# Kernel optimization log

Measured on AMD Instinct MI355X. Metric: run time of the kernel, lower is better.

Reference implementation:

```python
import jax, jax.numpy as jnp
import numpy as np

DIM = 1024
D_STATE = 16
D_CONV = 4
EXPAND = 2
D_INNER = EXPAND * DIM
BATCH = 4
SEQ = 2048


def setup_inputs() -> dict:
    key = jax.random.key(0)
    ks = jax.random.split(key, 9)
    n = lambda i, shape, scale=0.02: (jax.random.normal(ks[i], shape, jnp.float32) * scale)
    return {
        "x": jax.random.normal(ks[0], (BATCH, SEQ, DIM), jnp.float32),
        "in_proj_w": n(1, (D_INNER, DIM)),
        "conv_w": n(2, (D_INNER, D_CONV), 0.1),          # depthwise kernel (groups=d_inner)
        "x_proj_w": n(3, (2 * D_STATE + 1, D_INNER)),
        "dt_proj_w": n(4, (D_INNER, 1), 1.0),
        "dt_proj_b": n(5, (D_INNER,), 0.1),
        "A_log": jax.random.normal(ks[6], (D_INNER, D_STATE), jnp.float32),
        "D": jnp.ones((D_INNER,), jnp.float32),
        "out_proj_w": n(7, (DIM, D_INNER)),
        "norm_w": jnp.ones((DIM,), jnp.float32),
        "norm_b": jnp.zeros((DIM,), jnp.float32),
    }


def reference(x, in_proj_w, conv_w, x_proj_w, dt_proj_w, dt_proj_b,
              A_log, D, out_proj_w, norm_w, norm_b):
    Bsz, L, _ = x.shape
    shortcut = x

    # LayerNorm
    mu = jnp.mean(x, axis=-1, keepdims=True)
    var = jnp.var(x, axis=-1, keepdims=True)
    h = (x - mu) / jnp.sqrt(var + 1e-5) * norm_w + norm_b

    # in_proj: [B,L,dim] -> [B,L,d_inner]
    h = h @ in_proj_w.T

    # causal depthwise conv1d (padding d_conv-1, truncate to L)
    hp = jnp.pad(h, ((0, 0), (D_CONV - 1, 0), (0, 0)))
    h_conv = sum(hp[:, k:k + L, :] * conv_w[:, k] for k in range(D_CONV))
    h = jax.nn.silu(h_conv)

    # x_proj -> dt (1), B (d_state), C (d_state)
    proj = h @ x_proj_w.T
    dt_in = proj[..., :1]
    B_param = proj[..., 1:1 + D_STATE]      # [B,L,d_state]
    C_param = proj[..., 1 + D_STATE:]       # [B,L,d_state]
    dt = jax.nn.softplus(dt_in @ dt_proj_w.T + dt_proj_b)  # [B,L,d_inner]

    A = -jnp.exp(A_log)                     # [d_inner, d_state]

    def step(state, inp):
        dt_t, B_t, C_t, x_t = inp           # [B,d_inner],[B,ds],[B,ds],[B,d_inner]
        state = jnp.exp(A[None] * dt_t[:, :, None]) * state \
                + B_t[:, None, :] * x_t[:, :, None]          # [B,d_inner,d_state]
        y = jnp.einsum('bnd,bd->bn', state, C_t) + D * x_t   # [B,d_inner]
        return state, y

    init = jnp.zeros((Bsz, D_INNER, D_STATE), x.dtype)
    xs = (jnp.swapaxes(dt, 0, 1), jnp.swapaxes(B_param, 0, 1),
          jnp.swapaxes(C_param, 0, 1), jnp.swapaxes(h, 0, 1))
    state, ys = jax.lax.scan(step, init, xs)
    y = jnp.swapaxes(ys, 0, 1)              # [B,L,d_inner]

    out = jax.nn.silu(y) @ out_proj_w.T + shortcut
    return out, state
```

## Files before the change

### kernel.cpp

```cpp
#include <hip/hip_runtime.h>

typedef unsigned short u16;
typedef unsigned int u32;
typedef __attribute__((ext_vector_type(8))) short short8;
typedef __attribute__((ext_vector_type(4))) float f32x4;
typedef __attribute__((ext_vector_type(8))) unsigned short ushort8_t;

#define SEQ 2048
#define DIM 1024
#define DINNER 2048
#define NPROJ 33
#define NPROJ_PAD 48
#define LC 32
#define NC 64

__device__ __forceinline__ u16 f2bf(float f) {
  union { float f; u32 u; } v; v.f = f;
  u32 r = (v.u + 0x7fffu + ((v.u >> 16) & 1u)) >> 16;
  return (u16)r;
}
__device__ __forceinline__ float bf2f(u16 s) {
  union { u32 u; float f; } v; v.u = ((u32)s) << 16;
  return v.f;
}
__device__ __forceinline__ float fexp2(float x) {
#if __has_builtin(__builtin_amdgcn_exp2f)
  return __builtin_amdgcn_exp2f(x);
#else
  return __expf(x * 0.69314718f);
#endif
}
__device__ __forceinline__ float softplus(float x) {
  return fmaxf(x, 0.f) + __logf(1.f + __expf(-fabsf(x)));
}
__device__ __forceinline__ void async16(const void* g, void* l) {
  __builtin_amdgcn_global_load_lds(
      (const __attribute__((address_space(1))) u32*)g,
      (__attribute__((address_space(3))) u32*)l, 16, 0, 0);
}

__global__ void cast_w_kernel(const float* __restrict__ w1, const float* __restrict__ w3,
                              u16* __restrict__ o1, u16* __restrict__ o3) {
  int i = blockIdx.x * 256 + threadIdx.x;
  float4 a = ((const float4*)w1)[i];
  float4 b = ((const float4*)w3)[i];
  ushort4 oa, ob;
  oa.x = f2bf(a.x); oa.y = f2bf(a.y); oa.z = f2bf(a.z); oa.w = f2bf(a.w);
  ob.x = f2bf(b.x); ob.y = f2bf(b.y); ob.z = f2bf(b.z); ob.w = f2bf(b.w);
  ((ushort4*)o1)[i] = oa;
  ((ushort4*)o3)[i] = ob;
}

__global__ void cast_w2pad_kernel(const float* __restrict__ src, u16* __restrict__ dst) {
  int i = blockIdx.x * 256 + threadIdx.x;
  int j = i >> 11, k = i & 2047;
  dst[i] = (j < NPROJ) ? f2bf(src[j * 2048 + k]) : (u16)0;
}

__global__ __launch_bounds__(256) void ln_kernel(const float* __restrict__ x,
                                                 const float* __restrict__ w,
                                                 const float* __restrict__ b,
                                                 u16* __restrict__ h) {
  const int row = blockIdx.x;
  const int tid = threadIdx.x;
  const int lane = tid & 63, wave = tid >> 6;
  const float4 v = ((const float4*)(x + (size_t)row * DIM))[tid];
  float s = v.x + v.y + v.z + v.w;
  float q = v.x * v.x + v.y * v.y + v.z * v.z + v.w * v.w;
  for (int off = 32; off; off >>= 1) {
    s += __shfl_down(s, off);
    q += __shfl_down(q, off);
  }
  __shared__ float sbuf[8];
  if (lane == 0) { sbuf[wave] = s; sbuf[4 + wave] = q; }
  __syncthreads();
  float tot = sbuf[0] + sbuf[1] + sbuf[2] + sbuf[3];
  float totq = sbuf[4] + sbuf[5] + sbuf[6] + sbuf[7];
  const float mean = tot * (1.0f / DIM);
  const float var = totq * (1.0f / DIM) - mean * mean;
  const float rs = rsqrtf(var + 1e-5f);
  const float4 wv = ((const float4*)w)[tid];
  const float4 bv = ((const float4*)b)[tid];
  ushort4 o;
  o.x = f2bf((v.x - mean) * rs * wv.x + bv.x);
  o.y = f2bf((v.y - mean) * rs * wv.y + bv.y);
  o.z = f2bf((v.z - mean) * rs * wv.z + bv.z);
  o.w = f2bf((v.w - mean) * rs * wv.w + bv.w);
  ((ushort4*)(h + (size_t)row * DIM))[tid] = o;
}

__global__ __launch_bounds__(256) void gemm_bf16_kernel(const u16* __restrict__ A,
                                                        const u16* __restrict__ Bt,
                                                        u16* __restrict__ C,
                                                        int K, int N) {
  __shared__ u16 As[128 * 32];
  __shared__ u16 Bs[128 * 32];
  const int tid = threadIdx.x;
  const int lane = tid & 63, wave = tid >> 6;
  const int wm = wave >> 1, wn = wave & 1;
  const int row16 = lane & 15, quad = lane >> 4;
  const int bn = blockIdx.x, bm = blockIdx.y;
  f32x4 acc[4][4] = {};
  const u16* Ablk = A + (size_t)bm * 128 * K;
  const u16* Bblk = Bt + (size_t)bn * 128 * K;
  for (int k0 = 0; k0 < K; k0 += 32) {
#pragma unroll
    for (int i = 0; i < 2; ++i) {
      int c = tid + i * 256;
      int r = c >> 2, cc = (c & 3) * 8;
      async16(Ablk + (size_t)r * K + k0 + cc, &As[c * 8]);
      async16(Bblk + (size_t)r * K + k0 + cc, &Bs[c * 8]);
    }
    __syncthreads();
    short8 af[4], bfr[4];
#pragma unroll
    for (int i = 0; i < 4; ++i) {
      af[i] = *(const short8*)&As[(wm * 64 + i * 16 + row16) * 32 + quad * 8];
      bfr[i] = *(const short8*)&Bs[(wn * 64 + i * 16 + row16) * 32 + quad * 8];
    }
#pragma unroll
    for (int i = 0; i < 4; ++i)
#pragma unroll
      for (int j = 0; j < 4; ++j)
        acc[i][j] = __builtin_amdgcn_mfma_f32_16x16x32_bf16(af[i], bfr[j], acc[i][j], 0, 0, 0);
    __syncthreads();
  }
#pragma unroll
  for (int i = 0; i < 4; ++i) {
    int m = bm * 128 + wm * 64 + i * 16 + quad * 4;
#pragma unroll
    for (int j = 0; j < 4; ++j) {
      int n = bn * 128 + wn * 64 + j * 16 + row16;
#pragma unroll
      for (int r = 0; r < 4; ++r)
        C[(size_t)(m + r) * N + n] = f2bf(acc[i][j][r]);
    }
  }
}

__global__ __launch_bounds__(256) void gemm_out_kernel(const u16* __restrict__ A,
                                                       const u16* __restrict__ Bt,
                                                       const float* __restrict__ resid,
                                                       float* __restrict__ C,
                                                       int K, int N) {
  __shared__ u16 As[128 * 32];
  __shared__ u16 Bs[128 * 32];
  const int tid = threadIdx.x;
  const int lane = tid & 63, wave = tid >> 6;
  const int wm = wave >> 1, wn = wave & 1;
  const int row16 = lane & 15, quad = lane >> 4;
  const int bn = blockIdx.x, bm = blockIdx.y;
  f32x4 acc[4][4] = {};
  const u16* Ablk = A + (size_t)bm * 128 * K;
  const u16* Bblk = Bt + (size_t)bn * 128 * K;
  for (int k0 = 0; k0 < K; k0 += 32) {
#pragma unroll
    for (int i = 0; i < 2; ++i) {
      int c = tid + i * 256;
      int r = c >> 2, cc = (c & 3) * 8;
      async16(Ablk + (size_t)r * K + k0 + cc, &As[c * 8]);
      async16(Bblk + (size_t)r * K + k0 + cc, &Bs[c * 8]);
    }
    __syncthreads();
    short8 af[4], bfr[4];
#pragma unroll
    for (int i = 0; i < 4; ++i) {
      af[i] = *(const short8*)&As[(wm * 64 + i * 16 + row16) * 32 + quad * 8];
      bfr[i] = *(const short8*)&Bs[(wn * 64 + i * 16 + row16) * 32 + quad * 8];
    }
#pragma unroll
    for (int i = 0; i < 4; ++i)
#pragma unroll
      for (int j = 0; j < 4; ++j)
        acc[i][j] = __builtin_amdgcn_mfma_f32_16x16x32_bf16(af[i], bfr[j], acc[i][j], 0, 0, 0);
    __syncthreads();
  }
#pragma unroll
  for (int i = 0; i < 4; ++i) {
    int m = bm * 128 + wm * 64 + i * 16 + quad * 4;
#pragma unroll
    for (int j = 0; j < 4; ++j) {
      int n = bn * 128 + wn * 64 + j * 16 + row16;
#pragma unroll
      for (int r = 0; r < 4; ++r) {
        size_t idx = (size_t)(m + r) * N + n;
        C[idx] = acc[i][j][r] + resid[idx];
      }
    }
  }
}

__global__ __launch_bounds__(256) void conv_silu_kernel(const u16* __restrict__ c1,
                                                        const float* __restrict__ cw,
                                                        u16* __restrict__ cs) {
  const int tid = threadIdx.x;
  const int dg = tid * 8;
  const size_t m0 = (size_t)blockIdx.x * 8;
  const int l0 = (int)(m0 & (SEQ - 1));
  float w[4][8];
  {
    const float4* cw4 = (const float4*)(cw + (size_t)dg * 4);
#pragma unroll
    for (int c = 0; c < 8; ++c) {
      float4 v = cw4[c];
      w[0][c] = v.x; w[1][c] = v.y; w[2][c] = v.z; w[3][c] = v.w;
    }
  }
  const u16* base = c1 + m0 * DINNER + dg;
  ushort8_t win0, win1, win2, win3;
  const ushort8_t zero = (ushort8_t)0;
  if (l0 == 0) {
    win0 = zero; win1 = zero; win2 = zero;
  } else {
    win0 = *(const ushort8_t*)(base - 3 * DINNER);
    win1 = *(const ushort8_t*)(base - 2 * DINNER);
    win2 = *(const ushort8_t*)(base - 1 * DINNER);
  }
  win3 = *(const ushort8_t*)(base);
#pragma unroll
  for (int t = 0; t < 8; ++t) {
    ushort8_t nxt = win3;
    if (t < 7) nxt = *(const ushort8_t*)(base + (size_t)(t + 1) * DINNER);
    ushort8_t o;
#pragma unroll
    for (int c = 0; c < 8; ++c) {
      float acc = bf2f((u16)win0[c]) * w[0][c];
      acc = fmaf(bf2f((u16)win1[c]), w[1][c], acc);
      acc = fmaf(bf2f((u16)win2[c]), w[2][c], acc);
      acc = fmaf(bf2f((u16)win3[c]), w[3][c], acc);
      const float s = acc / (1.f + __expf(-acc));
      o[c] = (unsigned short)f2bf(s);
    }
    *(ushort8_t*)(cs + (m0 + t) * DINNER + dg) = o;
    win0 = win1; win1 = win2; win2 = win3; win3 = nxt;
  }
}

__global__ __launch_bounds__(256) void gemm_w2_kernel(const u16* __restrict__ A,
                                                      const u16* __restrict__ Bt,
                                                      float* __restrict__ C) {
  __shared__ u16 As[128 * 32];
  __shared__ u16 Bs[48 * 32];
  const int tid = threadIdx.x;
  const int lane = tid & 63, wave = tid >> 6;
  const int row16 = lane & 15, quad = lane >> 4;
  const int bm = blockIdx.x;
  const int K = DINNER;
  f32x4 acc[2][3] = {};
  const u16* Ablk = A + (size_t)bm * 128 * K;
  for (int k0 = 0; k0 < K; k0 += 32) {
#pragma unroll
    for (int i = 0; i < 2; ++i) {
      int c = tid + i * 256;
      int r = c >> 2, cc = (c & 3) * 8;
      async16(Ablk + (size_t)r * K + k0 + cc, &As[c * 8]);
    }
    if (tid < 192) {
      int c = tid;
      int r = c >> 2, cc = (c & 3) * 8;
      async16(Bt + (size_t)r * K + k0 + cc, &Bs[c * 8]);
    }
    __syncthreads();
    short8 af[2], bfr[3];
#pragma unroll
    for (int i = 0; i < 2; ++i)
      af[i] = *(const short8*)&As[(wave * 32 + i * 16 + row16) * 32 + quad * 8];
#pragma unroll
    for (int j = 0; j < 3; ++j)
      bfr[j] = *(const short8*)&Bs[(j * 16 + row16) * 32 + quad * 8];
#pragma unroll
    for (int i = 0; i < 2; ++i)
#pragma unroll
      for (int j = 0; j < 3; ++j)
        acc[i][j] = __builtin_amdgcn_mfma_f32_16x16x32_bf16(af[i], bfr[j], acc[i][j], 0, 0, 0);
    __syncthreads();
  }
#pragma unroll
  for (int i = 0; i < 2; ++i) {
    int m = bm * 128 + wave * 32 + i * 16 + quad * 4;
#pragma unroll
    for (int j = 0; j < 3; ++j) {
      int n = j * 16 + row16;
#pragma unroll
      for (int r = 0; r < 4; ++r)
        C[(size_t)(m + r) * NPROJ_PAD + n] = acc[i][j][r];
    }
  }
}


__global__ __launch_bounds__(256) void scan_phase1(const float* __restrict__ proj,
                                                   const u16* __restrict__ xs,
                                                   const float* __restrict__ dtw_,
                                                   const float* __restrict__ dtb_,
                                                   const float* __restrict__ A_log,
                                                   u16* __restrict__ S,
                                                   float* __restrict__ Tdt) {
  __shared__ float Bs[LC][16];
  __shared__ float DTin[LC];
  const int tid = threadIdx.x;
  const int d = blockIdx.x * 256 + tid;
  const int c = blockIdx.y;
  const int b = blockIdx.z;
  const size_t mrow = (size_t)b * SEQ + c * LC;
  for (int i = tid; i < LC * 16; i += 256) {
    int t = i >> 4, n = i & 15;
    Bs[t][n] = proj[(mrow + t) * NPROJ_PAD + 1 + n];
  }
  if (tid < LC) DTin[tid] = proj[(mrow + tid) * NPROJ_PAD];
  __syncthreads();
  float An2[16];
#pragma unroll
  for (int n = 0; n < 16; ++n) An2[n] = -__expf(A_log[d * 16 + n]) * 1.44269504f;
  const float dtw = dtw_[d], dtb = dtb_[d];
  float s[16];
#pragma unroll
  for (int n = 0; n < 16; ++n) s[n] = 0.f;
  float Tsum = 0.f;
  const u16* xp = xs + mrow * DINNER + d;
  u16 xnext = *xp;
#pragma unroll 2
  for (int t = 0; t < LC; ++t) {
    const float xv = bf2f(xnext);
    if (t + 1 < LC) xnext = xp[(size_t)(t + 1) * DINNER];
    const float sp = softplus(fmaf(DTin[t], dtw, dtb));
    Tsum += sp;
    const float4 B0 = *(const float4*)&Bs[t][0];
    const float4 B1 = *(const float4*)&Bs[t][4];
    const float4 B2 = *(const float4*)&Bs[t][8];
    const float4 B3 = *(const float4*)&Bs[t][12];
    const float bb[16] = {B0.x, B0.y, B0.z, B0.w, B1.x, B1.y, B1.z, B1.w,
                          B2.x, B2.y, B2.z, B2.w, B3.x, B3.y, B3.z, B3.w};
#pragma unroll
    for (int n = 0; n < 16; ++n)
      s[n] = fmaf(fexp2(An2[n] * sp), s[n], bb[n] * xv);
  }
  const size_t so = ((size_t)(b * NC + c) * DINNER + d) * 16;
  ushort8_t o0, o1;
#pragma unroll
  for (int j = 0; j < 8; ++j) {
    o0[j] = (unsigned short)f2bf(s[j]);
    o1[j] = (unsigned short)f2bf(s[8 + j]);
  }
  *(ushort8_t*)(S + so) = o0;
  *(ushort8_t*)(S + so + 8) = o1;
  Tdt[(size_t)(b * NC + c) * DINNER + d] = Tsum;
}

__global__ __launch_bounds__(256) void scan_phase2(const float* __restrict__ A_log,
                                                   u16* __restrict__ S,
                                                   const float* __restrict__ Tdt,
                                                   float* __restrict__ out_state) {
  const int idx = blockIdx.x * 256 + threadIdx.x;
  const int nq = idx & 3;
  const int d = (idx >> 2) & (DINNER - 1);
  const int b = idx >> 13;
  float An2[4];
#pragma unroll
  for (int n = 0; n < 4; ++n) An2[n] = -__expf(A_log[d * 16 + nq * 4 + n]) * 1.44269504f;
  float prev[4] = {0.f, 0.f, 0.f, 0.f};
  for (int c = 0; c < NC; ++c) {
    const size_t base = (size_t)(b * NC + c) * DINNER + d;
    const float T = Tdt[base];
    const size_t so = base * 16 + nq * 4;
    ushort4 lv = *(const ushort4*)(S + so);
    const float loc[4] = {bf2f(lv.x), bf2f(lv.y), bf2f(lv.z), bf2f(lv.w)};
    ushort4 pv;
    pv.x = f2bf(prev[0]); pv.y = f2bf(prev[1]); pv.z = f2bf(prev[2]); pv.w = f2bf(prev[3]);
    *(ushort4*)(S + so) = pv;
    const float dk = fexp2(An2[0] * T), dk1 = fexp2(An2[1] * T);
    const float dk2 = fexp2(An2[2] * T), dk3 = fexp2(An2[3] * T);
    prev[0] = fmaf(dk, prev[0], loc[0]);
    prev[1] = fmaf(dk1, prev[1], loc[1]);
    prev[2] = fmaf(dk2, prev[2], loc[2]);
    prev[3] = fmaf(dk3, prev[3], loc[3]);
  }
  *(float4*)(out_state + ((size_t)b * DINNER + d) * 16 + nq * 4) =
      make_float4(prev[0], prev[1], prev[2], prev[3]);
}

__global__ __launch_bounds__(256) void scan_phase3(const float* __restrict__ proj,
                                                   const u16* __restrict__ xs,
                                                   const float* __restrict__ dtw_,
                                                   const float* __restrict__ dtb_,
                                                   const float* __restrict__ A_log,
                                                   const float* __restrict__ Dp,
                                                   const u16* __restrict__ S,
                                                   u16* __restrict__ ysil) {
  __shared__ float Bs[LC][16];
  __shared__ float Cs[LC][16];
  __shared__ float DTin[LC];
  const int tid = threadIdx.x;
  const int d = blockIdx.x * 256 + tid;
  const int c = blockIdx.y;
  const int b = blockIdx.z;
  const size_t mrow = (size_t)b * SEQ + c * LC;
  for (int i = tid; i < LC * 16; i += 256) {
    int t = i >> 4, n = i & 15;
    Bs[t][n] = proj[(mrow + t) * NPROJ_PAD + 1 + n];
    Cs[t][n] = proj[(mrow + t) * NPROJ_PAD + 17 + n];
  }
  if (tid < LC) DTin[tid] = proj[(mrow + tid) * NPROJ_PAD];
  __syncthreads();
  float An2[16];
#pragma unroll
  for (int n = 0; n < 16; ++n) An2[n] = -__expf(A_log[d * 16 + n]) * 1.44269504f;
  const float dtw = dtw_[d], dtb = dtb_[d], Dd = Dp[d];
  float s[16];
  const size_t so = ((size_t)(b * NC + c) * DINNER + d) * 16;
  {
    ushort8_t v0 = *(const ushort8_t*)(S + so);
    ushort8_t v1 = *(const ushort8_t*)(S + so + 8);
#pragma unroll
    for (int j = 0; j < 8; ++j) {
      s[j] = bf2f((u16)v0[j]);
      s[8 + j] = bf2f((u16)v1[j]);
    }
  }
  const u16* xp = xs + mrow * DINNER + d;
  u16* yp = ysil + mrow * DINNER + d;
  u16 xnext = *xp;
#pragma unroll 2
  for (int t = 0; t < LC; ++t) {
    const float xv = bf2f(xnext);
    if (t + 1 < LC) xnext = xp[(size_t)(t + 1) * DINNER];
    const float sp = softplus(fmaf(DTin[t], dtw, dtb));
    const float4 B0 = *(const float4*)&Bs[t][0];
    const float4 B1 = *(const float4*)&Bs[t][4];
    const float4 B2 = *(const float4*)&Bs[t][8];
    const float4 B3 = *(const float4*)&Bs[t][12];
    const float bb[16] = {B0.x, B0.y, B0.z, B0.w, B1.x, B1.y, B1.z, B1.w,
                          B2.x, B2.y, B2.z, B2.w, B3.x, B3.y, B3.z, B3.w};
#pragma unroll
    for (int n = 0; n < 16; ++n)
      s[n] = fmaf(fexp2(An2[n] * sp), s[n], bb[n] * xv);
    const float4 C0 = *(const float4*)&Cs[t][0];
    const float4 C1 = *(const float4*)&Cs[t][4];
    const float4 C2 = *(const float4*)&Cs[t][8];
    const float4 C3 = *(const float4*)&Cs[t][12];
    const float cc[16] = {C0.x, C0.y, C0.z, C0.w, C1.x, C1.y, C1.z, C1.w,
                          C2.x, C2.y, C2.z, C2.w, C3.x, C3.y, C3.z, C3.w};
    float y = Dd * xv;
#pragma unroll
    for (int n = 0; n < 16; ++n) y = fmaf(cc[n], s[n], y);
    const float sy = y / (1.f + __expf(-y));
    yp[(size_t)t * DINNER] = f2bf(sy);
  }
}

extern "C" void kernel_launch(void* const* d_in, const int* in_sizes, int n_in,
                              void* d_out, int out_size, void* d_ws, size_t ws_size,
                              hipStream_t stream) {
  const float* x = (const float*)d_in[0];
  const float* in_proj_w = (const float*)d_in[1];
  const float* conv_w = (const float*)d_in[2];
  const float* x_proj_w = (const float*)d_in[3];
  const float* dt_proj_w = (const float*)d_in[4];
  const float* dt_proj_b = (const float*)d_in[5];
  const float* A_log = (const float*)d_in[6];
  const float* Dvec = (const float*)d_in[7];
  const float* out_proj_w = (const float*)d_in[8];
  const float* norm_w = (const float*)d_in[9];
  const float* norm_b = (const float*)d_in[10];

  char* ws = (char*)d_ws;
  u16* h = (u16*)(ws + 0);
  u16* w1b = (u16*)(ws + 16777216);
  u16* w3b = (u16*)(ws + 20971520);
  u16* w2b = (u16*)(ws + 25165824);
  u16* c1 = (u16*)(ws + 25362432);
  u16* ysil = c1;
  u16* cs = (u16*)(ws + 58916864);
  float* proj = (float*)(ws + 92471296);
  u16* Sbuf = (u16*)(ws + 94044160);
  float* Tdt = (float*)(ws + 110821376);

  float* out = (float*)d_out;
  float* out_state = out + (size_t)4 * SEQ * DIM;

  cast_w_kernel<<<2048, 256, 0, stream>>>(in_proj_w, out_proj_w, w1b, w3b);
  cast_w2pad_kernel<<<384, 256, 0, stream>>>(x_proj_w, w2b);
  ln_kernel<<<8192, 256, 0, stream>>>(x, norm_w, norm_b, h);
  gemm_bf16_kernel<<<dim3(DINNER / 128, 64), 256, 0, stream>>>(h, w1b, c1, DIM, DINNER);
  conv_silu_kernel<<<1024, 256, 0, stream>>>(c1, conv_w, cs);
  gemm_w2_kernel<<<64, 256, 0, stream>>>(cs, w2b, proj);
  scan_phase1<<<dim3(DINNER / 256, NC, 4), 256, 0, stream>>>(proj, cs, dt_proj_w, dt_proj_b,
                                                             A_log, Sbuf, Tdt);
  scan_phase2<<<128, 256, 0, stream>>>(A_log, Sbuf, Tdt, out_state);
  scan_phase3<<<dim3(DINNER / 256, NC, 4), 256, 0, stream>>>(proj, cs, dt_proj_w, dt_proj_b,
                                                             A_log, Dvec, Sbuf, ysil);
  gemm_out_kernel<<<dim3(DIM / 128, 64), 256, 0, stream>>>(ysil, w3b, x, out, DINNER, DIM);
}
```

Baseline: 395.4 us.

## Use 8-wave GEMM blocks, smaller x_proj tiles, and packed two-channel scan

The two large bf16 GEMMs now run 512 threads (8 waves) per 128x128 tile, each wave owning a 64x32 sub-tile. Each thread loads a single 16-byte chunk per stage, which is meant to improve latency hiding and occupancy. The skinny x_proj GEMM drops to 64-row tiles, doubling its block count to fill more CUs. The scan phase 1 and 3 kernels now handle two adjacent channels per thread with packed f32x2 FMAs and 32-bit paired bf16 loads and stores, which halves the number of blocks but aims to improve ALU throughput and memory access width.

Result: faster. 385.2 us (-2.6%).

```diff
diff --git a/kernel.cpp b/kernel.cpp
--- a/kernel.cpp
+++ b/kernel.cpp
@@ -4,6 +4,7 @@
 typedef unsigned int u32;
 typedef __attribute__((ext_vector_type(8))) short short8;
 typedef __attribute__((ext_vector_type(4))) float f32x4;
+typedef __attribute__((ext_vector_type(2))) float f32x2;
 typedef __attribute__((ext_vector_type(8))) unsigned short ushort8_t;
 
 #define SEQ 2048
@@ -23,6 +24,12 @@
   union { u32 u; float f; } v; v.u = ((u32)s) << 16;
   return v.f;
 }
+__device__ __forceinline__ float lo_bf(u32 w) {
+  union { u32 u; float f; } v; v.u = w << 16; return v.f;
+}
+__device__ __forceinline__ float hi_bf(u32 w) {
+  union { u32 u; float f; } v; v.u = w & 0xffff0000u; return v.f;
+}
 __device__ __forceinline__ float fexp2(float x) {
 #if __has_builtin(__builtin_amdgcn_exp2f)
   return __builtin_amdgcn_exp2f(x);
@@ -32,6 +39,10 @@
 }
 __device__ __forceinline__ float softplus(float x) {
   return fmaxf(x, 0.f) + __logf(1.f + __expf(-fabsf(x)));
+}
+__device__ __forceinline__ f32x2 sp2(float v) { f32x2 r; r.x = v; r.y = v; return r; }
+__device__ __forceinline__ f32x2 pkfma(f32x2 a, f32x2 b, f32x2 c) {
+  return __builtin_elementwise_fma(a, b, c);
 }
 __device__ __forceinline__ void async16(const void* g, void* l) {
   __builtin_amdgcn_global_load_lds(
@@ -89,7 +100,7 @@
   ((ushort4*)(h + (size_t)row * DIM))[tid] = o;
 }
 
-__global__ __launch_bounds__(256) void gemm_bf16_kernel(const u16* __restrict__ A,
+__global__ __launch_bounds__(512) void gemm_bf16_kernel(const u16* __restrict__ A,
                                                         const u16* __restrict__ Bt,
                                                         u16* __restrict__ C,
                                                         int K, int N) {
@@ -97,31 +108,28 @@
   __shared__ u16 Bs[128 * 32];
   const int tid = threadIdx.x;
   const int lane = tid & 63, wave = tid >> 6;
-  const int wm = wave >> 1, wn = wave & 1;
+  const int wm = wave >> 2, wn = wave & 3;
   const int row16 = lane & 15, quad = lane >> 4;
   const int bn = blockIdx.x, bm = blockIdx.y;
-  f32x4 acc[4][4] = {};
+  f32x4 acc[4][2] = {};
   const u16* Ablk = A + (size_t)bm * 128 * K;
   const u16* Bblk = Bt + (size_t)bn * 128 * K;
+  const int r = tid >> 2, cc = (tid & 3) * 8;
   for (int k0 = 0; k0 < K; k0 += 32) {
-#pragma unroll
-    for (int i = 0; i < 2; ++i) {
-      int c = tid + i * 256;
-      int r = c >> 2, cc = (c & 3) * 8;
-      async16(Ablk + (size_t)r * K + k0 + cc, &As[c * 8]);
-      async16(Bblk + (size_t)r * K + k0 + cc, &Bs[c * 8]);
-    }
+    async16(Ablk + (size_t)r * K + k0 + cc, &As[tid * 8]);
+    async16(Bblk + (size_t)r * K + k0 + cc, &Bs[tid * 8]);
     __syncthreads();
-    short8 af[4], bfr[4];
-#pragma unroll
-    for (int i = 0; i < 4; ++i) {
+    short8 af[4], bfr[2];
+#pragma unroll
+    for (int i = 0; i < 4; ++i)
       af[i] = *(const short8*)&As[(wm * 64 + i * 16 + row16) * 32 + quad * 8];
-      bfr[i] = *(const short8*)&Bs[(wn * 64 + i * 16 + row16) * 32 + quad * 8];
-    }
+#pragma unroll
+    for (int j = 0; j < 2; ++j)
+      bfr[j] = *(const short8*)&Bs[(wn * 32 + j * 16 + row16) * 32 + quad * 8];
 #pragma unroll
     for (int i = 0; i < 4; ++i)
 #pragma unroll
-      for (int j = 0; j < 4; ++j)
+      for (int j = 0; j < 2; ++j)
         acc[i][j] = __builtin_amdgcn_mfma_f32_16x16x32_bf16(af[i], bfr[j], acc[i][j], 0, 0, 0);
     __syncthreads();
   }
@@ -129,16 +137,16 @@
   for (int i = 0; i < 4; ++i) {
     int m = bm * 128 + wm * 64 + i * 16 + quad * 4;
 #pragma unroll
-    for (int j = 0; j < 4; ++j) {
-      int n = bn * 128 + wn * 64 + j * 16 + row16;
-#pragma unroll
-      for (int r = 0; r < 4; ++r)
-        C[(size_t)(m + r) * N + n] = f2bf(acc[i][j][r]);
-    }
-  }
-}
-
-__global__ __launch_bounds__(256) void gemm_out_kernel(const u16* __restrict__ A,
+    for (int j = 0; j < 2; ++j) {
+      int n = bn * 128 + wn * 32 + j * 16 + row16;
+#pragma unroll
+      for (int rr = 0; rr < 4; ++rr)
+        C[(size_t)(m + rr) * N + n] = f2bf(acc[i][j][rr]);
+    }
+  }
+}
+
+__global__ __launch_bounds__(512) void gemm_out_kernel(const u16* __restrict__ A,
                                                        const u16* __restrict__ Bt,
                                                        const float* __restrict__ resid,
                                                        float* __restrict__ C,
@@ -147,31 +155,28 @@
   __shared__ u16 Bs[128 * 32];
   const int tid = threadIdx.x;
   const int lane = tid & 63, wave = tid >> 6;
-  const int wm = wave >> 1, wn = wave & 1;
+  const int wm = wave >> 2, wn = wave & 3;
   const int row16 = lane & 15, quad = lane >> 4;
   const int bn = blockIdx.x, bm = blockIdx.y;
-  f32x4 acc[4][4] = {};
+  f32x4 acc[4][2] = {};
   const u16* Ablk = A + (size_t)bm * 128 * K;
   const u16* Bblk = Bt + (size_t)bn * 128 * K;
+  const int r = tid >> 2, cc = (tid & 3) * 8;
   for (int k0 = 0; k0 < K; k0 += 32) {
-#pragma unroll
-    for (int i = 0; i < 2; ++i) {
-      int c = tid + i * 256;
-      int r = c >> 2, cc = (c & 3) * 8;
-      async16(Ablk + (size_t)r * K + k0 + cc, &As[c * 8]);
-      async16(Bblk + (size_t)r * K + k0 + cc, &Bs[c * 8]);
-    }
+    async16(Ablk + (size_t)r * K + k0 + cc, &As[tid * 8]);
+    async16(Bblk + (size_t)r * K + k0 + cc, &Bs[tid * 8]);
     __syncthreads();
-    short8 af[4], bfr[4];
-#pragma unroll
-    for (int i = 0; i < 4; ++i) {
+    short8 af[4], bfr[2];
+#pragma unroll
+    for (int i = 0; i < 4; ++i)
       af[i] = *(const short8*)&As[(wm * 64 + i * 16 + row16) * 32 + quad * 8];
-      bfr[i] = *(const short8*)&Bs[(wn * 64 + i * 16 + row16) * 32 + quad * 8];
-    }
+#pragma unroll
+    for (int j = 0; j < 2; ++j)
+      bfr[j] = *(const short8*)&Bs[(wn * 32 + j * 16 + row16) * 32 + quad * 8];
 #pragma unroll
     for (int i = 0; i < 4; ++i)
 #pragma unroll
-      for (int j = 0; j < 4; ++j)
+      for (int j = 0; j < 2; ++j)
         acc[i][j] = __builtin_amdgcn_mfma_f32_16x16x32_bf16(af[i], bfr[j], acc[i][j], 0, 0, 0);
     __syncthreads();
   }
@@ -179,12 +184,12 @@
   for (int i = 0; i < 4; ++i) {
     int m = bm * 128 + wm * 64 + i * 16 + quad * 4;
 #pragma unroll
-    for (int j = 0; j < 4; ++j) {
-      int n = bn * 128 + wn * 64 + j * 16 + row16;
-#pragma unroll
-      for (int r = 0; r < 4; ++r) {
-        size_t idx = (size_t)(m + r) * N + n;
-        C[idx] = acc[i][j][r] + resid[idx];
+    for (int j = 0; j < 2; ++j) {
+      int n = bn * 128 + wn * 32 + j * 16 + row16;
+#pragma unroll
+      for (int rr = 0; rr < 4; ++rr) {
+        size_t idx = (size_t)(m + rr) * N + n;
+        C[idx] = acc[i][j][rr] + resid[idx];
       }
     }
   }
@@ -239,52 +244,37 @@
 __global__ __launch_bounds__(256) void gemm_w2_kernel(const u16* __restrict__ A,
                                                       const u16* __restrict__ Bt,
                                                       float* __restrict__ C) {
-  __shared__ u16 As[128 * 32];
+  __shared__ u16 As[64 * 32];
   __shared__ u16 Bs[48 * 32];
   const int tid = threadIdx.x;
   const int lane = tid & 63, wave = tid >> 6;
   const int row16 = lane & 15, quad = lane >> 4;
   const int bm = blockIdx.x;
   const int K = DINNER;
-  f32x4 acc[2][3] = {};
-  const u16* Ablk = A + (size_t)bm * 128 * K;
+  f32x4 acc[3] = {};
+  const u16* Ablk = A + (size_t)bm * 64 * K;
+  const int r = tid >> 2, cc = (tid & 3) * 8;
   for (int k0 = 0; k0 < K; k0 += 32) {
-#pragma unroll
-    for (int i = 0; i < 2; ++i) {
-      int c = tid + i * 256;
-      int r = c >> 2, cc = (c & 3) * 8;
-      async16(Ablk + (size_t)r * K + k0 + cc, &As[c * 8]);
-    }
-    if (tid < 192) {
-      int c = tid;
-      int r = c >> 2, cc = (c & 3) * 8;
-      async16(Bt + (size_t)r * K + k0 + cc, &Bs[c * 8]);
-    }
+    async16(Ablk + (size_t)r * K + k0 + cc, &As[tid * 8]);
+    if (tid < 192) async16(Bt + (size_t)r * K + k0 + cc, &Bs[tid * 8]);
     __syncthreads();
-    short8 af[2], bfr[3];
-#pragma unroll
-    for (int i = 0; i < 2; ++i)
-      af[i] = *(const short8*)&As[(wave * 32 + i * 16 + row16) * 32 + quad * 8];
+    short8 af = *(const short8*)&As[(wave * 16 + row16) * 32 + quad * 8];
+    short8 bfr[3];
 #pragma unroll
     for (int j = 0; j < 3; ++j)
       bfr[j] = *(const short8*)&Bs[(j * 16 + row16) * 32 + quad * 8];
 #pragma unroll
-    for (int i = 0; i < 2; ++i)
-#pragma unroll
-      for (int j = 0; j < 3; ++j)
-        acc[i][j] = __builtin_amdgcn_mfma_f32_16x16x32_bf16(af[i], bfr[j], acc[i][j], 0, 0, 0);
+    for (int j = 0; j < 3; ++j)
+      acc[j] = __builtin_amdgcn_mfma_f32_16x16x32_bf16(af, bfr[j], acc[j], 0, 0, 0);
     __syncthreads();
   }
-#pragma unroll
-  for (int i = 0; i < 2; ++i) {
-    int m = bm * 128 + wave * 32 + i * 16 + quad * 4;
-#pragma unroll
-    for (int j = 0; j < 3; ++j) {
-      int n = j * 16 + row16;
-#pragma unroll
-      for (int r = 0; r < 4; ++r)
-        C[(size_t)(m + r) * NPROJ_PAD + n] = acc[i][j][r];
-    }
+  const int m = bm * 64 + wave * 16 + quad * 4;
+#pragma unroll
+  for (int j = 0; j < 3; ++j) {
+    const int n = j * 16 + row16;
+#pragma unroll
+    for (int rr = 0; rr < 4; ++rr)
+      C[(size_t)(m + rr) * NPROJ_PAD + n] = acc[j][rr];
   }
 }
 
@@ -296,55 +286,66 @@
                                                    const float* __restrict__ A_log,
                                                    u16* __restrict__ S,
                                                    float* __restrict__ Tdt) {
-  __shared__ float Bs[LC][16];
+  __shared__ float Bsh[LC][16];
   __shared__ float DTin[LC];
   const int tid = threadIdx.x;
-  const int d = blockIdx.x * 256 + tid;
+  const int d0 = blockIdx.x * 512 + tid * 2;
   const int c = blockIdx.y;
   const int b = blockIdx.z;
   const size_t mrow = (size_t)b * SEQ + c * LC;
   for (int i = tid; i < LC * 16; i += 256) {
     int t = i >> 4, n = i & 15;
-    Bs[t][n] = proj[(mrow + t) * NPROJ_PAD + 1 + n];
+    Bsh[t][n] = proj[(mrow + t) * NPROJ_PAD + 1 + n];
   }
   if (tid < LC) DTin[tid] = proj[(mrow + tid) * NPROJ_PAD];
   __syncthreads();
-  float An2[16];
-#pragma unroll
-  for (int n = 0; n < 16; ++n) An2[n] = -__expf(A_log[d * 16 + n]) * 1.44269504f;
-  const float dtw = dtw_[d], dtb = dtb_[d];
-  float s[16];
-#pragma unroll
-  for (int n = 0; n < 16; ++n) s[n] = 0.f;
-  float Tsum = 0.f;
-  const u16* xp = xs + mrow * DINNER + d;
-  u16 xnext = *xp;
+  f32x2 An2[16];
+#pragma unroll
+  for (int n = 0; n < 16; ++n) {
+    An2[n].x = -__expf(A_log[(size_t)d0 * 16 + n]) * 1.44269504f;
+    An2[n].y = -__expf(A_log[(size_t)(d0 + 1) * 16 + n]) * 1.44269504f;
+  }
+  const float2 dtwv = *(const float2*)(dtw_ + d0);
+  const float2 dtbv = *(const float2*)(dtb_ + d0);
+  f32x2 dtw2; dtw2.x = dtwv.x; dtw2.y = dtwv.y;
+  f32x2 dtb2; dtb2.x = dtbv.x; dtb2.y = dtbv.y;
+  f32x2 s[16];
+#pragma unroll
+  for (int n = 0; n < 16; ++n) s[n] = sp2(0.f);
+  f32x2 Tsum = sp2(0.f);
+  const u16* xp = xs + mrow * DINNER + d0;
+  u32 xw = *(const u32*)xp;
 #pragma unroll 2
   for (int t = 0; t < LC; ++t) {
-    const float xv = bf2f(xnext);
-    if (t + 1 < LC) xnext = xp[(size_t)(t + 1) * DINNER];
-    const float sp = softplus(fmaf(DTin[t], dtw, dtb));
+    f32x2 xv; xv.x = lo_bf(xw); xv.y = hi_bf(xw);
+    if (t + 1 < LC) xw = *(const u32*)(xp + (size_t)(t + 1) * DINNER);
+    f32x2 dtv = pkfma(sp2(DTin[t]), dtw2, dtb2);
+    f32x2 sp; sp.x = softplus(dtv.x); sp.y = softplus(dtv.y);
     Tsum += sp;
-    const float4 B0 = *(const float4*)&Bs[t][0];
-    const float4 B1 = *(const float4*)&Bs[t][4];
-    const float4 B2 = *(const float4*)&Bs[t][8];
-    const float4 B3 = *(const float4*)&Bs[t][12];
-    const float bb[16] = {B0.x, B0.y, B0.z, B0.w, B1.x, B1.y, B1.z, B1.w,
-                          B2.x, B2.y, B2.z, B2.w, B3.x, B3.y, B3.z, B3.w};
-#pragma unroll
-    for (int n = 0; n < 16; ++n)
-      s[n] = fmaf(fexp2(An2[n] * sp), s[n], bb[n] * xv);
-  }
-  const size_t so = ((size_t)(b * NC + c) * DINNER + d) * 16;
-  ushort8_t o0, o1;
+    const float4* Br = (const float4*)&Bsh[t][0];
+#pragma unroll
+    for (int q = 0; q < 4; ++q) {
+      const float4 Bq = Br[q];
+      const float bqa[4] = {Bq.x, Bq.y, Bq.z, Bq.w};
+#pragma unroll
+      for (int j = 0; j < 4; ++j) {
+        const int n = q * 4 + j;
+        f32x2 e = An2[n] * sp;
+        f32x2 dk; dk.x = fexp2(e.x); dk.y = fexp2(e.y);
+        s[n] = pkfma(dk, s[n], sp2(bqa[j]) * xv);
+      }
+    }
+  }
+  const size_t so = ((size_t)(b * NC + c) * DINNER + d0) * 16;
+  ushort8_t o0, o1, o2, o3;
 #pragma unroll
   for (int j = 0; j < 8; ++j) {
-    o0[j] = (unsigned short)f2bf(s[j]);
-    o1[j] = (unsigned short)f2bf(s[8 + j]);
-  }
-  *(ushort8_t*)(S + so) = o0;
-  *(ushort8_t*)(S + so + 8) = o1;
-  Tdt[(size_t)(b * NC + c) * DINNER + d] = Tsum;
+    o0[j] = f2bf(s[j].x);     o1[j] = f2bf(s[8 + j].x);
+    o2[j] = f2bf(s[j].y);     o3[j] = f2bf(s[8 + j].y);
+  }
+  *(ushort8_t*)(S + so) = o0;       *(ushort8_t*)(S + so + 8) = o1;
+  *(ushort8_t*)(S + so + 16) = o2;  *(ushort8_t*)(S + so + 24) = o3;
+  *(float2*)(Tdt + (size_t)(b * NC + c) * DINNER + d0) = make_float2(Tsum.x, Tsum.y);
 }
 
 __global__ __launch_bounds__(256) void scan_phase2(const float* __restrict__ A_log,
@@ -368,9 +369,9 @@
     ushort4 pv;
     pv.x = f2bf(prev[0]); pv.y = f2bf(prev[1]); pv.z = f2bf(prev[2]); pv.w = f2bf(prev[3]);
     *(ushort4*)(S + so) = pv;
-    const float dk = fexp2(An2[0] * T), dk1 = fexp2(An2[1] * T);
+    const float dk0 = fexp2(An2[0] * T), dk1 = fexp2(An2[1] * T);
     const float dk2 = fexp2(An2[2] * T), dk3 = fexp2(An2[3] * T);
-    prev[0] = fmaf(dk, prev[0], loc[0]);
+    prev[0] = fmaf(dk0, prev[0], loc[0]);
     prev[1] = fmaf(dk1, prev[1], loc[1]);
     prev[2] = fmaf(dk2, prev[2], loc[2]);
     prev[3] = fmaf(dk3, prev[3], loc[3]);
@@ -387,64 +388,77 @@
                                                    const float* __restrict__ Dp,
                                                    const u16* __restrict__ S,
                                                    u16* __restrict__ ysil) {
-  __shared__ float Bs[LC][16];
-  __shared__ float Cs[LC][16];
+  __shared__ float Bsh[LC][16];
+  __shared__ float Csh[LC][16];
   __shared__ float DTin[LC];
   const int tid = threadIdx.x;
-  const int d = blockIdx.x * 256 + tid;
+  const int d0 = blockIdx.x * 512 + tid * 2;
   const int c = blockIdx.y;
   const int b = blockIdx.z;
   const size_t mrow = (size_t)b * SEQ + c * LC;
   for (int i = tid; i < LC * 16; i += 256) {
     int t = i >> 4, n = i & 15;
-    Bs[t][n] = proj[(mrow + t) * NPROJ_PAD + 1 + n];
-    Cs[t][n] = proj[(mrow + t) * NPROJ_PAD + 17 + n];
+    Bsh[t][n] = proj[(mrow + t) * NPROJ_PAD + 1 + n];
+    Csh[t][n] = proj[(mrow + t) * NPROJ_PAD + 17 + n];
   }
   if (tid < LC) DTin[tid] = proj[(mrow + tid) * NPROJ_PAD];
   __syncthreads();
-  float An2[16];
-#pragma unroll
-  for (int n = 0; n < 16; ++n) An2[n] = -__expf(A_log[d * 16 + n]) * 1.44269504f;
-  const float dtw = dtw_[d], dtb = dtb_[d], Dd = Dp[d];
-  float s[16];
-  const size_t so = ((size_t)(b * NC + c) * DINNER + d) * 16;
+  f32x2 An2[16];
+#pragma unroll
+  for (int n = 0; n < 16; ++n) {
+    An2[n].x = -__expf(A_log[(size_t)d0 * 16 + n]) * 1.44269504f;
+    An2[n].y = -__expf(A_log[(size_t)(d0 + 1) * 16 + n]) * 1.44269504f;
+  }
+  const float2 dtwv = *(const float2*)(dtw_ + d0);
+  const float2 dtbv = *(const float2*)(dtb_ + d0);
+  const float2 Ddv = *(const float2*)(Dp + d0);
+  f32x2 dtw2; dtw2.x = dtwv.x; dtw2.y = dtwv.y;
+  f32x2 dtb2; dtb2.x = dtbv.x; dtb2.y = dtbv.y;
+  f32x2 Dd2; Dd2.x = Ddv.x; Dd2.y = Ddv.y;
+  f32x2 s[16];
+  const size_t so = ((size_t)(b * NC + c) * DINNER + d0) * 16;
   {
     ushort8_t v0 = *(const ushort8_t*)(S + so);
     ushort8_t v1 = *(const ushort8_t*)(S + so + 8);
+    ushort8_t v2 = *(const ushort8_t*)(S + so + 16);
+    ushort8_t v3 = *(const ushort8_t*)(S + so + 24);
 #pragma unroll
     for (int j = 0; j < 8; ++j) {
-      s[j] = bf2f((u16)v0[j]);
-      s[8 + j] = bf2f((u16)v1[j]);
-    }
-  }
-  const u16* xp = xs + mrow * DINNER + d;
-  u16* yp = ysil + mrow * DINNER + d;
-  u16 xnext = *xp;
+      s[j].x = bf2f((u16)v0[j]);     s[8 + j].x = bf2f((u16)v1[j]);
+      s[j].y = bf2f((u16)v2[j]);     s[8 + j].y = bf2f((u16)v3[j]);
+    }
+  }
+  const u16* xp = xs + mrow * DINNER + d0;
+  u16* yp = ysil + mrow * DINNER + d0;
+  u32 xw = *(const u32*)xp;
 #pragma unroll 2
   for (int t = 0; t < LC; ++t) {
-    const float xv = bf2f(xnext);
-    if (t + 1 < LC) xnext = xp[(size_t)(t + 1) * DINNER];
-    const float sp = softplus(fmaf(DTin[t], dtw, dtb));
-    const float4 B0 = *(const float4*)&Bs[t][0];
-    const float4 B1 = *(const float4*)&Bs[t][4];
-    const float4 B2 = *(const float4*)&Bs[t][8];
-    const float4 B3 = *(const float4*)&Bs[t][12];
-    const float bb[16] = {B0.x, B0.y, B0.z, B0.w, B1.x, B1.y, B1.z, B1.w,
-                          B2.x, B2.y, B2.z, B2.w, B3.x, B3.y, B3.z, B3.w};
-#pragma unroll
-    for (int n = 0; n < 16; ++n)
-      s[n] = fmaf(fexp2(An2[n] * sp), s[n], bb[n] * xv);
-    const float4 C0 = *(const float4*)&Cs[t][0];
-    const float4 C1 = *(const float4*)&Cs[t][4];
-    const float4 C2 = *(const float4*)&Cs[t][8];
-    const float4 C3 = *(const float4*)&Cs[t][12];
-    const float cc[16] = {C0.x, C0.y, C0.z, C0.w, C1.x, C1.y, C1.z, C1.w,
-                          C2.x, C2.y, C2.z, C2.w, C3.x, C3.y, C3.z, C3.w};
-    float y = Dd * xv;
-#pragma unroll
-    for (int n = 0; n < 16; ++n) y = fmaf(cc[n], s[n], y);
-    const float sy = y / (1.f + __expf(-y));
-    yp[(size_t)t * DINNER] = f2bf(sy);
+    f32x2 xv; xv.x = lo_bf(xw); xv.y = hi_bf(xw);
+    if (t + 1 < LC) xw = *(const u32*)(xp + (size_t)(t + 1) * DINNER);
+    f32x2 dtv = pkfma(sp2(DTin[t]), dtw2, dtb2);
+    f32x2 sp; sp.x = softplus(dtv.x); sp.y = softplus(dtv.y);
+    f32x2 y = Dd2 * xv;
+    const float4* Br = (const float4*)&Bsh[t][0];
+    const float4* Cr = (const float4*)&Csh[t][0];
+#pragma unroll
+    for (int q = 0; q < 4; ++q) {
+      const float4 Bq = Br[q];
+      const float4 Cq = Cr[q];
+      const float bqa[4] = {Bq.x, Bq.y, Bq.z, Bq.w};
+      const float cqa[4] = {Cq.x, Cq.y, Cq.z, Cq.w};
+#pragma unroll
+      for (int j = 0; j < 4; ++j) {
+        const int n = q * 4 + j;
+        f32x2 e = An2[n] * sp;
+        f32x2 dk; dk.x = fexp2(e.x); dk.y = fexp2(e.y);
+        s[n] = pkfma(dk, s[n], sp2(bqa[j]) * xv);
+        y = pkfma(sp2(cqa[j]), s[n], y);
+      }
+    }
+    const float sy0 = y.x / (1.f + __expf(-y.x));
+    const float sy1 = y.y / (1.f + __expf(-y.y));
+    const u32 ow = (u32)f2bf(sy0) | ((u32)f2bf(sy1) << 16);
+    *(u32*)(yp + (size_t)t * DINNER) = ow;
   }
 }
 
@@ -481,13 +495,13 @@
   cast_w_kernel<<<2048, 256, 0, stream>>>(in_proj_w, out_proj_w, w1b, w3b);
   cast_w2pad_kernel<<<384, 256, 0, stream>>>(x_proj_w, w2b);
   ln_kernel<<<8192, 256, 0, stream>>>(x, norm_w, norm_b, h);
-  gemm_bf16_kernel<<<dim3(DINNER / 128, 64), 256, 0, stream>>>(h, w1b, c1, DIM, DINNER);
+  gemm_bf16_kernel<<<dim3(DINNER / 128, 64), 512, 0, stream>>>(h, w1b, c1, DIM, DINNER);
   conv_silu_kernel<<<1024, 256, 0, stream>>>(c1, conv_w, cs);
-  gemm_w2_kernel<<<64, 256, 0, stream>>>(cs, w2b, proj);
-  scan_phase1<<<dim3(DINNER / 256, NC, 4), 256, 0, stream>>>(proj, cs, dt_proj_w, dt_proj_b,
+  gemm_w2_kernel<<<128, 256, 0, stream>>>(cs, w2b, proj);
+  scan_phase1<<<dim3(DINNER / 512, NC, 4), 256, 0, stream>>>(proj, cs, dt_proj_w, dt_proj_b,
                                                              A_log, Sbuf, Tdt);
   scan_phase2<<<128, 256, 0, stream>>>(A_log, Sbuf, Tdt, out_state);
-  scan_phase3<<<dim3(DINNER / 256, NC, 4), 256, 0, stream>>>(proj, cs, dt_proj_w, dt_proj_b,
+  scan_phase3<<<dim3(DINNER / 512, NC, 4), 256, 0, stream>>>(proj, cs, dt_proj_w, dt_proj_b,
                                                              A_log, Dvec, Sbuf, ysil);
-  gemm_out_kernel<<<dim3(DIM / 128, 64), 256, 0, stream>>>(ysil, w3b, x, out, DINNER, DIM);
-}
+  gemm_out_kernel<<<dim3(DIM / 128, 64), 512, 0, stream>>>(ysil, w3b, x, out, DINNER, DIM);
+}
```
